# Optimization experiments

Measured on AMD Instinct MI355X. Metric: run time of the kernel, lower is better.

The kernel has to match this reference:

```python
import jax, jax.numpy as jnp
import numpy as np

N_DST = 50000
N_SRC = 50000
E = 800000
D = 128
R = 3
H_SEM = 128
NEG_SLOPE = 0.2  # DGL GATConv default


def setup_inputs() -> dict:
    key = jax.random.key(0)
    ks = jax.random.split(key, 40)
    s = 1.0 / np.sqrt(D)
    inp = {
        'dst_feat': jax.random.normal(ks[0], (N_DST, D), jnp.float32),
        'src_feat0': jax.random.normal(ks[1], (N_SRC, D), jnp.float32),
        'src_feat1': jax.random.normal(ks[2], (N_SRC, D), jnp.float32),
        'src_feat2': jax.random.normal(ks[3], (N_SRC, D), jnp.float32),
        'sem_W1': jax.random.normal(ks[4], (D, H_SEM), jnp.float32) * s,
        'sem_b1': jnp.zeros((H_SEM,), jnp.float32),
        'sem_W2': jax.random.normal(ks[5], (H_SEM, 1), jnp.float32) * (1.0 / np.sqrt(H_SEM)),
    }
    for r in range(R):
        inp[f'Wg{r}'] = jax.random.normal(ks[6 + r], (D, D), jnp.float32) * s
        inp[f'al{r}'] = jax.random.normal(ks[9 + r], (D,), jnp.float32) * s
        inp[f'ar{r}'] = jax.random.normal(ks[12 + r], (D,), jnp.float32) * s
        inp[f'bg{r}'] = jnp.zeros((D,), jnp.float32)
        inp[f'src_idx{r}'] = jax.random.randint(ks[15 + r], (E,), 0, N_SRC, jnp.int32)
        inp[f'dst_idx{r}'] = jax.random.randint(ks[18 + r], (E,), 0, N_DST, jnp.int32)
    return inp


def _gat(fs, fd, W, al, ar, b, sidx, didx):
    # DGL GATConv, num_heads=1, bipartite, eval mode (no dropout)
    hs = fs @ W                    # [Ns, D]
    hd = fd @ W                    # [Nd, D]
    el = hs @ al                   # [Ns]
    er = hd @ ar                   # [Nd]
    e = jax.nn.leaky_relu(el[sidx] + er[didx], NEG_SLOPE)  # [E]
    # edge softmax over incoming edges of each dst node
    m = jax.ops.segment_max(e, didx, num_segments=N_DST)
    a = jnp.exp(e - m[didx])
    z = jax.ops.segment_sum(a, didx, num_segments=N_DST)
    alpha = a / z[didx]            # [E]
    out = jax.ops.segment_sum(hs[sidx] * alpha[:, None], didx, num_segments=N_DST)
    return jax.nn.elu(out + b)     # [Nd, D]


def reference(dst_feat, src_feat0, src_feat1, src_feat2,
              Wg0, Wg1, Wg2, al0, al1, al2, ar0, ar1, ar2, bg0, bg1, bg2,
              sem_W1, sem_b1, sem_W2,
              src_idx0, src_idx1, src_idx2, dst_idx0, dst_idx1, dst_idx2):
    z0 = _gat(src_feat0, dst_feat, Wg0, al0, ar0, bg0, src_idx0, dst_idx0)
    z1 = _gat(src_feat1, dst_feat, Wg1, al1, ar1, bg1, src_idx1, dst_idx1)
    z2 = _gat(src_feat2, dst_feat, Wg2, al2, ar2, bg2, src_idx2, dst_idx2)
    z_m = jnp.stack([z0, z1, z2], axis=1)            # [N, R, D]
    h = jnp.tanh(z_m @ sem_W1 + sem_b1) @ sem_W2     # [N, R, 1]
    w = h.mean(axis=0)                               # [R, 1]
    a_w = jax.nn.softmax(w, axis=0)                  # [R, 1]
    z = (z_m * a_w[None, :, :]).sum(axis=1)          # [N, D]
    att_mp = a_w.squeeze()                           # [R]
    return (z, att_mp)
```

## Files before the change

kernel.cpp:

```cpp
#include <hip/hip_runtime.h>
#include <math.h>

#define D_DIM 128
#define N_DST 50000
#define N_SRC 50000
#define NE    800000
#define NEG_SLOPE 0.2f

#define NB        196
#define CAP       4608
#define CHUNK     8192
#define NBLK_REL  98
#define GEMM_BLKS 196
#define GEMM_GRID (3 * GEMM_BLKS)
#define ER_PB     86
#define SEM_GRID  512
#define SEM_TILES ((3 * N_DST + 63) / 64)

typedef unsigned short ushort_t;
using f32x4  = __attribute__((ext_vector_type(4))) float;
using bf16x8 = __attribute__((ext_vector_type(8))) short;

__device__ __forceinline__ ushort_t f2bf(float x) {
    unsigned u = __float_as_uint(x);
    unsigned r = (u + 0x7fffu + ((u >> 16) & 1u)) >> 16;
    return (ushort_t)r;
}
__device__ __forceinline__ float bf2f(ushort_t b) {
    return __uint_as_float(((unsigned)b) << 16);
}
__device__ __forceinline__ float bflo(unsigned u) { return __uint_as_float(u << 16); }
__device__ __forceinline__ float bfhi(unsigned u) { return __uint_as_float(u & 0xffff0000u); }
__device__ __forceinline__ float tanh_fast(float x) {
    float e = __expf(2.f * x);
    return 1.f - 2.f / (e + 1.f);
}

__device__ __forceinline__ void cvt8(float4 f0, float4 f1, bf16x8& hi, bf16x8& lo) {
    float f[8] = {f0.x, f0.y, f0.z, f0.w, f1.x, f1.y, f1.z, f1.w};
    #pragma unroll
    for (int i = 0; i < 8; i++) {
        ushort_t h = f2bf(f[i]);
        hi[i] = (short)h;
        lo[i] = (short)(ushort_t)(__float_as_uint(f[i] - bf2f(h)) >> 16);
    }
}

__global__ __launch_bounds__(256) void vecprep_kernel(
        const float* __restrict__ Wg0, const float* __restrict__ Wg1,
        const float* __restrict__ Wg2,
        const float* __restrict__ ar0, const float* __restrict__ ar1,
        const float* __restrict__ ar2,
        const float* __restrict__ W1,
        float* __restrict__ wv, ushort_t* __restrict__ Wt_g,
        ushort_t* __restrict__ Bv) {
    int bx = blockIdx.x, tid = threadIdx.x;
    if (bx < 3) {
        if (tid < 128) {
            const float* W  = bx == 0 ? Wg0 : (bx == 1 ? Wg1 : Wg2);
            const float* ar = bx == 0 ? ar0 : (bx == 1 ? ar1 : ar2);
            float sar = 0.f;
            for (int j = 0; j < D_DIM; j++) sar = fmaf(W[tid * D_DIM + j], ar[j], sar);
            wv[bx * D_DIM + tid] = sar;
        }
    } else if (bx < 67) {
        int idx = (bx - 3) * 256 + tid;
        int k = idx >> 7, n = idx & 127;
        Wt_g[n * 128 + k] = f2bf(W1[idx]);
    } else {
        int q = bx - 67;
        int rel = q >> 6;
        int idx = (q & 63) * 256 + tid;
        const float* W = rel == 0 ? Wg0 : (rel == 1 ? Wg1 : Wg2);
        int k = idx >> 7, n = idx & 127;
        float v = W[idx];
        ushort_t hi = f2bf(v);
        ushort_t lo = f2bf(v - bf2f(hi));
        int nt = n >> 4, l15 = n & 15;
        int kc = k >> 5, quad = (k >> 3) & 3, e = k & 7;
        int h2 = nt >> 2, n4 = nt & 3;
        int lane = quad * 16 + l15;
        int fh = kc * 16 + h2 * 8 + n4;
        ushort_t* dst = Bv + (size_t)rel * 32768;
        dst[(fh)     * 512 + lane * 8 + e] = hi;
        dst[(fh + 4) * 512 + lane * 8 + e] = lo;
    }
}

__global__ __launch_bounds__(256) void bucket_scatter_kernel(
        const int* __restrict__ d0, const int* __restrict__ d1, const int* __restrict__ d2,
        const int* __restrict__ s0, const int* __restrict__ s1, const int* __restrict__ s2,
        int* __restrict__ bucketCur, int2* __restrict__ pairs) {
    __shared__ int cnt[NB], base[NB], cur[NB];
    int bx = blockIdx.x;
    int r = bx / NBLK_REL, blk = bx % NBLK_REL;
    const int* dd = r == 0 ? d0 : (r == 1 ? d1 : d2);
    const int* ss = r == 0 ? s0 : (r == 1 ? s1 : s2);
    int tid = threadIdx.x;
    if (tid < NB) { cnt[tid] = 0; cur[tid] = 0; }
    __syncthreads();
    int e0 = blk * CHUNK, e1 = min(e0 + CHUNK, NE);
    for (int e = e0 + tid; e < e1; e += 256) atomicAdd(&cnt[dd[e] >> 8], 1);
    __syncthreads();
    if (tid < NB) base[tid] = cnt[tid] ? atomicAdd(&bucketCur[r * NB + tid], cnt[tid]) : 0;
    __syncthreads();
    for (int e = e0 + tid; e < e1; e += 256) {
        int d = dd[e], b = d >> 8;
        int rank = atomicAdd(&cur[b], 1);
        pairs[(size_t)(r * NB + b) * CAP + base[b] + rank] = make_int2(ss[e], d);
    }
}

__global__ __launch_bounds__(256) void csr_kernel(
        const int2* __restrict__ pairs, const int* __restrict__ bucketCur,
        int* __restrict__ offs, int* __restrict__ cnts, int* __restrict__ perm) {
    __shared__ int hist[256], sc[256], cur[256];
    int bx = blockIdx.x;
    int r = bx / NB, b = bx % NB;
    int tid = threadIdx.x;
    int nE = bucketCur[r * NB + b];
    size_t region = (size_t)(r * NB + b) * CAP;
    const int2* pr = pairs + region;
    hist[tid] = 0;
    __syncthreads();
    for (int i = tid; i < nE; i += 256) atomicAdd(&hist[pr[i].y & 255], 1);
    __syncthreads();
    int v = hist[tid];
    sc[tid] = v;
    __syncthreads();
    for (int off = 1; off < 256; off <<= 1) {
        int t = tid >= off ? sc[tid - off] : 0;
        __syncthreads();
        sc[tid] += t;
        __syncthreads();
    }
    int excl = sc[tid] - v;
    int dstg = b * 256 + tid;
    if (dstg < N_DST) { offs[r * N_DST + dstg] = (int)region + excl; cnts[r * N_DST + dstg] = v; }
    cur[tid] = excl;
    __syncthreads();
    int* pm = perm + region;
    for (int i = tid; i < nE; i += 256) {
        int2 p = pr[i];
        int rank = atomicAdd(&cur[p.y & 255], 1);
        pm[rank] = p.x;
    }
}

__global__ __launch_bounds__(512) void gemm_er_kernel(
        const float* __restrict__ A0, const float* __restrict__ A1, const float* __restrict__ A2,
        const ushort_t* __restrict__ Bv,
        const float* __restrict__ al0, const float* __restrict__ al1, const float* __restrict__ al2,
        const float* __restrict__ dstf, const float* __restrict__ wv,
        ushort_t* __restrict__ hs, float* __restrict__ elv) {
    __shared__ ushort_t Bs[32768];
    int bx = blockIdx.x;
    int rel = bx / GEMM_BLKS, blk = bx % GEMM_BLKS;
    const float* A  = rel == 0 ? A0 : (rel == 1 ? A1 : A2);
    const float* al = rel == 0 ? al0 : (rel == 1 ? al1 : al2);
    ushort_t* C = hs + (size_t)rel * N_SRC * 128;
    int tid = threadIdx.x;

    {
        const uint4* src = (const uint4*)(Bv + (size_t)rel * 32768);
        uint4* dl = (uint4*)Bs;
        #pragma unroll
        for (int i = 0; i < 8; i++) dl[tid + i * 512] = src[tid + i * 512];
    }

    int w = tid >> 6, lane = tid & 63;
    int quad = lane >> 4, l15 = lane & 15;
    int row0 = blk * 256 + w * 32;

    int gr0 = row0 + l15;      if (gr0 > N_SRC - 1) gr0 = N_SRC - 1;
    int gr1 = row0 + 16 + l15; if (gr1 > N_SRC - 1) gr1 = N_SRC - 1;
    const float* a0p = A + (size_t)gr0 * 128 + quad * 8;
    const float* a1p = A + (size_t)gr1 * 128 + quad * 8;

    float4 abuf[2][2][2];
    abuf[0][0][0] = *(const float4*)(a0p + 0);
    abuf[0][0][1] = *(const float4*)(a0p + 4);
    abuf[0][1][0] = *(const float4*)(a1p + 0);
    abuf[0][1][1] = *(const float4*)(a1p + 4);

    __syncthreads();

    f32x4 acc[2][8] = {};
    #pragma unroll
    for (int kc = 0; kc < 4; kc++) {
        const int par = kc & 1;
        if (kc < 3) {
            int ko = (kc + 1) * 32;
            abuf[par ^ 1][0][0] = *(const float4*)(a0p + ko);
            abuf[par ^ 1][0][1] = *(const float4*)(a0p + ko + 4);
            abuf[par ^ 1][1][0] = *(const float4*)(a1p + ko);
            abuf[par ^ 1][1][1] = *(const float4*)(a1p + ko + 4);
        }
        bf16x8 ah[2], alo[2];
        #pragma unroll
        for (int t = 0; t < 2; t++)
            cvt8(abuf[par][t][0], abuf[par][t][1], ah[t], alo[t]);

        #pragma unroll
        for (int h2 = 0; h2 < 2; h2++) {
            #pragma unroll
            for (int n4 = 0; n4 < 4; n4++) {
                int f = kc * 16 + h2 * 8 + n4;
                bf16x8 bh = *(const bf16x8*)&Bs[f * 512 + lane * 8];
                bf16x8 bl = *(const bf16x8*)&Bs[(f + 4) * 512 + lane * 8];
                int nt = h2 * 4 + n4;
                #pragma unroll
                for (int t = 0; t < 2; t++) {
                    acc[t][nt] = __builtin_amdgcn_mfma_f32_16x16x32_bf16(ah[t],  bh, acc[t][nt], 0, 0, 0);
                    acc[t][nt] = __builtin_amdgcn_mfma_f32_16x16x32_bf16(alo[t], bh, acc[t][nt], 0, 0, 0);
                    acc[t][nt] = __builtin_amdgcn_mfma_f32_16x16x32_bf16(ah[t],  bl, acc[t][nt], 0, 0, 0);
                }
            }
        }
    }

    float alv[8];
    #pragma unroll
    for (int nt = 0; nt < 8; nt++) alv[nt] = al[nt * 16 + l15];
    #pragma unroll
    for (int t = 0; t < 2; t++) {
        float part[4] = {0.f, 0.f, 0.f, 0.f};
        #pragma unroll
        for (int nt = 0; nt < 8; nt++)
            #pragma unroll
            for (int i = 0; i < 4; i++)
                part[i] = fmaf(acc[t][nt][i], alv[nt], part[i]);
        #pragma unroll
        for (int msk = 1; msk < 16; msk <<= 1)
            #pragma unroll
            for (int i = 0; i < 4; i++) part[i] += __shfl_xor(part[i], msk);
        if (l15 == 0) {
            #pragma unroll
            for (int i = 0; i < 4; i++) {
                int gr = row0 + t * 16 + quad * 4 + i;
                if (gr < N_SRC) elv[rel * N_DST + gr] = part[i];
            }
        }
    }

    int erbase = bx * ER_PB;
    float m0[11], m1[11];
    float wl0 = 0.f, wh0 = 0.f, wl1 = 0.f, wh1 = 0.f, wl2 = 0.f, wh2 = 0.f;
    int rend = 0;
    if (erbase < N_DST) {
        rend = min(erbase + ER_PB, N_DST);
        wl0 = wv[lane];       wh0 = wv[lane + 64];
        wl1 = wv[128 + lane]; wh1 = wv[128 + lane + 64];
        wl2 = wv[256 + lane]; wh2 = wv[256 + lane + 64];
        #pragma unroll
        for (int j = 0; j < 11; j++) {
            int r = erbase + w + 8 * j;
            int rr = r < rend ? r : erbase;
            m0[j] = dstf[(size_t)rr * 128 + lane];
            m1[j] = dstf[(size_t)rr * 128 + lane + 64];
        }
    }

    __syncthreads();

    ushort_t* Csh = Bs + w * 2304;
    #pragma unroll
    for (int h = 0; h < 2; h++) {
        __asm__ __volatile__("" ::: "memory");
        #pragma unroll
        for (int t = 0; t < 2; t++)
            #pragma unroll
            for (int ntl = 0; ntl < 4; ntl++) {
                int nt = h * 4 + ntl;
                #pragma unroll
                for (int i = 0; i < 4; i++)
                    Csh[(t * 16 + quad * 4 + i) * 72 + ntl * 16 + l15] = f2bf(acc[t][nt][i]);
            }
        __asm__ __volatile__("" ::: "memory");
        int r2 = lane >> 1, cb = (lane & 1) * 32;
        int gr = row0 + r2;
        if (gr < N_SRC) {
            ushort_t* dst = C + (size_t)gr * 128 + h * 64 + cb;
            #pragma unroll
            for (int k2 = 0; k2 < 4; k2++) {
                uint4 v = *(const uint4*)&Csh[r2 * 72 + cb + k2 * 8];
                *(uint4*)(dst + k2 * 8) = v;
            }
        }
    }

    if (erbase < N_DST) {
        #pragma unroll
        for (int j = 0; j < 11; j++) {
            int r = erbase + w + 8 * j;
            if (r < rend) {
                float p0 = fmaf(m0[j], wl0, m1[j] * wh0);
                float p1 = fmaf(m0[j], wl1, m1[j] * wh1);
                float p2 = fmaf(m0[j], wl2, m1[j] * wh2);
                #pragma unroll
                for (int off = 32; off > 0; off >>= 1) {
                    p0 += __shfl_down(p0, off);
                    p1 += __shfl_down(p1, off);
                    p2 += __shfl_down(p2, off);
                }
                if (lane == 0) {
                    elv[3 * N_DST + r] = p0;
                    elv[4 * N_DST + r] = p1;
                    elv[5 * N_DST + r] = p2;
                }
            }
        }
    }
}

__global__ __launch_bounds__(256) void aggregate_kernel(
        const ushort_t* __restrict__ hs, const float* __restrict__ elv,
        const int* __restrict__ perm, const int* __restrict__ offs,
        const int* __restrict__ cnts,
        const float* __restrict__ bg0, const float* __restrict__ bg1,
        const float* __restrict__ bg2, float* __restrict__ zm) {
    __shared__ int2 ew[4][2][64];
    int tid = threadIdx.x;
    int wave = tid >> 6, lane = tid & 63;
    int hw = lane >> 5, l31 = lane & 31;
    int bx  = blockIdx.x;
    int rel = bx / 6250;
    int b   = (bx % 6250) * 8 + wave * 2 + hw;
    const float* el  = elv + rel * N_DST;
    float erb = elv[(3 + rel) * N_DST + b];
    const float* bg = rel == 0 ? bg0 : (rel == 1 ? bg1 : bg2);
    const ushort_t* hsr = hs + (size_t)rel * N_SRC * 128;
    int o0 = offs[rel * N_DST + b], deg = cnts[rel * N_DST + b];
    float* zout = zm + ((size_t)b * 3 + rel) * 128;
    int2* ews = ew[wave][hw];

    if (deg <= 64) {
        int s0 = 0, s1 = 0;
        float e0 = 0.f, e1 = 0.f;
        if (l31 < deg) {
            s0 = perm[o0 + l31];
            float x = el[s0] + erb;
            x = x >= 0.f ? x : NEG_SLOPE * x;
            e0 = __expf(x);
        }
        if (deg > 32 && l31 + 32 < deg) {
            s1 = perm[o0 + l31 + 32];
            float x = el[s1] + erb;
            x = x >= 0.f ? x : NEG_SLOPE * x;
            e1 = __expf(x);
        }
        float lsum = e0 + e1;
        #pragma unroll
        for (int msk = 1; msk < 32; msk <<= 1) lsum += __shfl_xor(lsum, msk);
        float invz = deg > 0 ? 1.f / lsum : 0.f;

        ews[l31] = make_int2(s0 * 256, __float_as_int(e0 * invz));
        if (deg > 32)
            ews[l31 + 32] = make_int2(s1 * 256, __float_as_int(e1 * invz));
        __asm__ __volatile__("" ::: "memory");

        int degp = (deg + 3) & ~3;
        const char* basep = (const char*)hsr;
        int sub = l31 >> 4;
        int col16 = (l31 & 15) * 16;
        float a0 = 0.f, a1 = 0.f, a2 = 0.f, a3 = 0.f;
        float a4 = 0.f, a5 = 0.f, a6 = 0.f, a7 = 0.f;
        for (int j = 0; j < degp; j += 4) {
            int2 pA = ews[j + sub];
            int2 pB = ews[j + 2 + sub];
            uint4 hA = *(const uint4*)(basep + (unsigned)(pA.x + col16));
            uint4 hB = *(const uint4*)(basep + (unsigned)(pB.x + col16));
            float eA = __int_as_float(pA.y), eB = __int_as_float(pB.y);
            a0 = fmaf(eA, bflo(hA.x), a0); a1 = fmaf(eA, bfhi(hA.x), a1);
            a2 = fmaf(eA, bflo(hA.y), a2); a3 = fmaf(eA, bfhi(hA.y), a3);
            a4 = fmaf(eA, bflo(hA.z), a4); a5 = fmaf(eA, bfhi(hA.z), a5);
            a6 = fmaf(eA, bflo(hA.w), a6); a7 = fmaf(eA, bfhi(hA.w), a7);
            a0 = fmaf(eB, bflo(hB.x), a0); a1 = fmaf(eB, bfhi(hB.x), a1);
            a2 = fmaf(eB, bflo(hB.y), a2); a3 = fmaf(eB, bfhi(hB.y), a3);
            a4 = fmaf(eB, bflo(hB.z), a4); a5 = fmaf(eB, bfhi(hB.z), a5);
            a6 = fmaf(eB, bflo(hB.w), a6); a7 = fmaf(eB, bfhi(hB.w), a7);
        }
        a0 += __shfl_xor(a0, 16); a1 += __shfl_xor(a1, 16);
        a2 += __shfl_xor(a2, 16); a3 += __shfl_xor(a3, 16);
        a4 += __shfl_xor(a4, 16); a5 += __shfl_xor(a5, 16);
        a6 += __shfl_xor(a6, 16); a7 += __shfl_xor(a7, 16);
        if (sub == 0) {
            int c = (l31 & 15) * 8;
            float4 bgv0 = *(const float4*)&bg[c];
            float4 bgv1 = *(const float4*)&bg[c + 4];
            float4 z0, z1;
            z0.x = a0 + bgv0.x; z0.y = a1 + bgv0.y;
            z0.z = a2 + bgv0.z; z0.w = a3 + bgv0.w;
            z1.x = a4 + bgv1.x; z1.y = a5 + bgv1.y;
            z1.z = a6 + bgv1.z; z1.w = a7 + bgv1.w;
            z0.x = z0.x > 0.f ? z0.x : __expf(z0.x) - 1.f;
            z0.y = z0.y > 0.f ? z0.y : __expf(z0.y) - 1.f;
            z0.z = z0.z > 0.f ? z0.z : __expf(z0.z) - 1.f;
            z0.w = z0.w > 0.f ? z0.w : __expf(z0.w) - 1.f;
            z1.x = z1.x > 0.f ? z1.x : __expf(z1.x) - 1.f;
            z1.y = z1.y > 0.f ? z1.y : __expf(z1.y) - 1.f;
            z1.z = z1.z > 0.f ? z1.z : __expf(z1.z) - 1.f;
            z1.w = z1.w > 0.f ? z1.w : __expf(z1.w) - 1.f;
            *(float4*)&zout[c] = z0;
            *(float4*)&zout[c + 4] = z1;
        }
    } else {
        float lmax = -INFINITY;
        for (int i = l31; i < deg; i += 32) {
            int s = perm[o0 + i];
            float x = el[s] + erb;
            x = x >= 0.f ? x : NEG_SLOPE * x;
            lmax = fmaxf(lmax, x);
        }
        #pragma unroll
        for (int msk = 1; msk < 32; msk <<= 1) lmax = fmaxf(lmax, __shfl_xor(lmax, msk));
        float lsum = 0.f;
        for (int i = l31; i < deg; i += 32) {
            int s = perm[o0 + i];
            float x = el[s] + erb;
            x = x >= 0.f ? x : NEG_SLOPE * x;
            lsum += __expf(x - lmax);
        }
        #pragma unroll
        for (int msk = 1; msk < 32; msk <<= 1) lsum += __shfl_xor(lsum, msk);
        float invz = 1.f / lsum;
        float c0 = 0.f, c1 = 0.f, c2 = 0.f, c3 = 0.f;
        for (int j = 0; j < deg; j++) {
            int s = perm[o0 + j];
            float x = el[s] + erb;
            x = x >= 0.f ? x : NEG_SLOPE * x;
            float e_ = __expf(x - lmax) * invz;
            uint2 hv = *(const uint2*)(hsr + (size_t)s * 128 + l31 * 4);
            c0 = fmaf(e_, bflo(hv.x), c0);
            c1 = fmaf(e_, bfhi(hv.x), c1);
            c2 = fmaf(e_, bflo(hv.y), c2);
            c3 = fmaf(e_, bfhi(hv.y), c3);
        }
        int c = l31 * 4;
        float4 bgv = *(const float4*)&bg[c];
        float4 z;
        z.x = c0 + bgv.x; z.y = c1 + bgv.y;
        z.z = c2 + bgv.z; z.w = c3 + bgv.w;
        z.x = z.x > 0.f ? z.x : __expf(z.x) - 1.f;
        z.y = z.y > 0.f ? z.y : __expf(z.y) - 1.f;
        z.z = z.z > 0.f ? z.z : __expf(z.z) - 1.f;
        z.w = z.w > 0.f ? z.w : __expf(z.w) - 1.f;
        *(float4*)&zout[c] = z;
    }
}

__global__ __launch_bounds__(256) void semantic_kernel(
        const float* __restrict__ zm, const ushort_t* __restrict__ Wt_g,
        const float* __restrict__ b1, const float* __restrict__ W2,
        float* __restrict__ w_sum) {
    __shared__ ushort_t Wt[128 * 136];
    __shared__ float hsum[3];
    const int NROWS = N_DST * 3;
    int tid = threadIdx.x;
    if (tid < 3) hsum[tid] = 0.f;

    #pragma unroll
    for (int i = 0; i < 8; i++) {
        int c = i * 256 + tid;
        int n = c >> 4, c16 = c & 15;
        uint4 t = *(const uint4*)(Wt_g + n * 128 + c16 * 8);
        *(uint4*)&Wt[n * 136 + c16 * 8] = t;
    }
    __syncthreads();

    int w    = tid >> 6, lane = tid & 63;
    int quad = lane >> 4, l15 = lane & 15;
    float bb = b1[l15 * 8 + 0];

    for (int tile = blockIdx.x; tile < SEM_TILES; tile += gridDim.x) {
        long row0 = (long)tile * 64 + w * 16;
        long rA = row0 + l15; if (rA > NROWS - 1) rA = NROWS - 1;

        f32x4 acc[8] = {};
        #pragma unroll
        for (int kc = 0; kc < 4; kc++) {
            int k0 = kc * 32 + quad * 8;
            const float* src = zm + (size_t)rA * 128 + k0;
            float4 f0 = *(const float4*)src;
            float4 f1 = *(const float4*)(src + 4);
            bf16x8 a;
            a[0] = (short)f2bf(f0.x); a[1] = (short)f2bf(f0.y);
            a[2] = (short)f2bf(f0.z); a[3] = (short)f2bf(f0.w);
            a[4] = (short)f2bf(f1.x); a[5] = (short)f2bf(f1.y);
            a[6] = (short)f2bf(f1.z); a[7] = (short)f2bf(f1.w);
            #pragma unroll
            for (int nt = 0; nt < 8; nt++) {
                int n = nt * 16 + l15;
                bf16x8 bfr = *(const bf16x8*)&Wt[n * 136 + k0];
                acc[nt] = __builtin_amdgcn_mfma_f32_16x16x32_bf16(a, bfr, acc[nt], 0, 0, 0);
            }
        }

        float part[4] = {0.f, 0.f, 0.f, 0.f};
        #pragma unroll
        for (int nt = 0; nt < 8; nt++) {
            int n = nt * 16 + l15;
            float bbn = b1[n], ww = W2[n];
            #pragma unroll
            for (int i = 0; i < 4; i++) {
                float t = tanh_fast(acc[nt][i] + bbn);
                part[i] = fmaf(t, ww, part[i]);
            }
        }
        #pragma unroll
        for (int msk = 1; msk < 16; msk <<= 1)
            #pragma unroll
            for (int i = 0; i < 4; i++) part[i] += __shfl_xor(part[i], msk);
        if (l15 == 0) {
            #pragma unroll
            for (int i = 0; i < 4; i++) {
                long R = row0 + quad * 4 + i;
                if (R < NROWS) atomicAdd(&hsum[(int)(R % 3)], part[i]);
            }
        }
    }
    __syncthreads();
    if (tid < 3) atomicAdd(&w_sum[tid], hsum[tid]);
    (void)bb;
}

__global__ void combine_kernel(const float* __restrict__ zm, const float* __restrict__ w_sum,
                               float* __restrict__ out, float* __restrict__ out_att) {
    float w0 = w_sum[0] * (1.f / (float)N_DST);
    float w1 = w_sum[1] * (1.f / (float)N_DST);
    float w2 = w_sum[2] * (1.f / (float)N_DST);
    float m = fmaxf(w0, fmaxf(w1, w2));
    float e0 = __expf(w0 - m), e1 = __expf(w1 - m), e2 = __expf(w2 - m);
    float s = 1.f / (e0 + e1 + e2);
    float a0 = e0 * s, a1 = e1 * s, a2 = e2 * s;
    if (blockIdx.x == 0 && threadIdx.x < 3)
        out_att[threadIdx.x] = threadIdx.x == 0 ? a0 : (threadIdx.x == 1 ? a1 : a2);
    int id4 = blockIdx.x * 256 + threadIdx.x;
    int n  = id4 >> 5;
    int d4 = (id4 & 31) * 4;
    const float4 z0 = *(const float4*)&zm[((size_t)n * 3 + 0) * 128 + d4];
    const float4 z1 = *(const float4*)&zm[((size_t)n * 3 + 1) * 128 + d4];
    const float4 z2 = *(const float4*)&zm[((size_t)n * 3 + 2) * 128 + d4];
    float4 o;
    o.x = a0 * z0.x + a1 * z1.x + a2 * z2.x;
    o.y = a0 * z0.y + a1 * z1.y + a2 * z2.y;
    o.z = a0 * z0.z + a1 * z1.z + a2 * z2.z;
    o.w = a0 * z0.w + a1 * z1.w + a2 * z2.w;
    *(float4*)&out[(size_t)n * 128 + d4] = o;
}

extern "C" void kernel_launch(void* const* d_in, const int* in_sizes, int n_in,
                              void* d_out, int out_size, void* d_ws, size_t ws_size,
                              hipStream_t stream) {
    const float* dstf   = (const float*)d_in[0];
    const float* src0   = (const float*)d_in[1];
    const float* src1   = (const float*)d_in[2];
    const float* src2   = (const float*)d_in[3];
    const float* sem_W1 = (const float*)d_in[4];
    const float* sem_b1 = (const float*)d_in[5];
    const float* sem_W2 = (const float*)d_in[6];
    const float* Wg[3]  = {(const float*)d_in[7],  (const float*)d_in[13], (const float*)d_in[19]};
    const float* al[3]  = {(const float*)d_in[8],  (const float*)d_in[14], (const float*)d_in[20]};
    const float* ar[3]  = {(const float*)d_in[9],  (const float*)d_in[15], (const float*)d_in[21]};
    const float* bg[3]  = {(const float*)d_in[10], (const float*)d_in[16], (const float*)d_in[22]};
    const int*  sidx[3] = {(const int*)d_in[11], (const int*)d_in[17], (const int*)d_in[23]};
    const int*  didx[3] = {(const int*)d_in[12], (const int*)d_in[18], (const int*)d_in[24]};
    float* out = (float*)d_out;

    char* p = (char*)d_ws;
    auto alloc = [&](size_t bytes) -> char* {
        char* q = p; p += (bytes + 255) & ~(size_t)255; return q;
    };
    float*    zm   = (float*)alloc((size_t)N_DST * 3 * 128 * 4);
    ushort_t* hs   = (ushort_t*)alloc((size_t)3 * N_SRC * 128 * 2);
    float*    elv  = (float*)alloc((size_t)6 * N_DST * 4);
    float*    wv   = (float*)alloc((size_t)3 * 128 * 4);
    ushort_t* Wt_g = (ushort_t*)alloc((size_t)128 * 128 * 2);
    ushort_t* Bv   = (ushort_t*)alloc((size_t)3 * 32768 * 2);
    int* cnts = (int*)alloc((size_t)3 * N_DST * 4);
    int* offs = (int*)alloc((size_t)3 * N_DST * 4);
    int* perm = (int*)alloc((size_t)3 * NB * CAP * 4);
    int* zero = (int*)alloc((size_t)(3 * NB + 8) * 4);
    int*   bucketCur = zero;
    float* wsum      = (float*)(zero + 3 * NB);
    int2* pairs = (int2*)zm;

    hipMemsetAsync(zero, 0, (size_t)(3 * NB + 8) * 4, stream);

    vecprep_kernel<<<259, 256, 0, stream>>>(Wg[0], Wg[1], Wg[2], ar[0], ar[1], ar[2],
                                            sem_W1, wv, Wt_g, Bv);
    bucket_scatter_kernel<<<3 * NBLK_REL, 256, 0, stream>>>(didx[0], didx[1], didx[2],
                                                            sidx[0], sidx[1], sidx[2],
                                                            bucketCur, pairs);
    csr_kernel<<<3 * NB, 256, 0, stream>>>(pairs, bucketCur, offs, cnts, perm);
    gemm_er_kernel<<<GEMM_GRID, 512, 0, stream>>>(src0, src1, src2, Bv,
                                                  al[0], al[1], al[2],
                                                  dstf, wv, hs, elv);
    aggregate_kernel<<<3 * 6250, 256, 0, stream>>>(hs, elv, perm, offs, cnts,
                                                   bg[0], bg[1], bg[2], zm);
    semantic_kernel<<<SEM_GRID, 256, 0, stream>>>(zm, Wt_g, sem_b1, sem_W2, wsum);
    combine_kernel<<<6250, 256, 0, stream>>>(zm, wsum, out, out + (size_t)N_DST * 128);
}
```

Measured before the change: 417.7 us.

## Merge independent prep/scatter and CSR/GEMM kernels into shared launches

Combines the weight-prep and edge bucket-scatter kernels into one launch via block-index dispatch, and runs the CSR build blocks alongside the feature GEMM blocks in a single launch. This removes two kernel launch boundaries and lets independent work overlap on the GPU. The CSR path now runs with 512-thread blocks sharing the GEMM's LDS allocation, so its blocks carry the GEMM's large shared-memory footprint, which may limit occupancy.

```diff
diff --git a/kernel.cpp b/kernel.cpp
--- a/kernel.cpp
+++ b/kernel.cpp
@@ -13,6 +13,7 @@
 #define NBLK_REL  98
 #define GEMM_BLKS 196
 #define GEMM_GRID (3 * GEMM_BLKS)
+#define CSR_GRID  (3 * NB)
 #define ER_PB     86
 #define SEM_GRID  512
 #define SEM_TILES ((3 * N_DST + 63) / 64)
@@ -46,57 +47,56 @@
     }
 }
 
-__global__ __launch_bounds__(256) void vecprep_kernel(
+__global__ __launch_bounds__(256) void prep_scatter_kernel(
         const float* __restrict__ Wg0, const float* __restrict__ Wg1,
         const float* __restrict__ Wg2,
         const float* __restrict__ ar0, const float* __restrict__ ar1,
         const float* __restrict__ ar2,
         const float* __restrict__ W1,
         float* __restrict__ wv, ushort_t* __restrict__ Wt_g,
-        ushort_t* __restrict__ Bv) {
-    int bx = blockIdx.x, tid = threadIdx.x;
-    if (bx < 3) {
-        if (tid < 128) {
-            const float* W  = bx == 0 ? Wg0 : (bx == 1 ? Wg1 : Wg2);
-            const float* ar = bx == 0 ? ar0 : (bx == 1 ? ar1 : ar2);
-            float sar = 0.f;
-            for (int j = 0; j < D_DIM; j++) sar = fmaf(W[tid * D_DIM + j], ar[j], sar);
-            wv[bx * D_DIM + tid] = sar;
-        }
-    } else if (bx < 67) {
-        int idx = (bx - 3) * 256 + tid;
-        int k = idx >> 7, n = idx & 127;
-        Wt_g[n * 128 + k] = f2bf(W1[idx]);
-    } else {
-        int q = bx - 67;
-        int rel = q >> 6;
-        int idx = (q & 63) * 256 + tid;
-        const float* W = rel == 0 ? Wg0 : (rel == 1 ? Wg1 : Wg2);
-        int k = idx >> 7, n = idx & 127;
-        float v = W[idx];
-        ushort_t hi = f2bf(v);
-        ushort_t lo = f2bf(v - bf2f(hi));
-        int nt = n >> 4, l15 = n & 15;
-        int kc = k >> 5, quad = (k >> 3) & 3, e = k & 7;
-        int h2 = nt >> 2, n4 = nt & 3;
-        int lane = quad * 16 + l15;
-        int fh = kc * 16 + h2 * 8 + n4;
-        ushort_t* dst = Bv + (size_t)rel * 32768;
-        dst[(fh)     * 512 + lane * 8 + e] = hi;
-        dst[(fh + 4) * 512 + lane * 8 + e] = lo;
-    }
-}
-
-__global__ __launch_bounds__(256) void bucket_scatter_kernel(
+        ushort_t* __restrict__ Bv,
         const int* __restrict__ d0, const int* __restrict__ d1, const int* __restrict__ d2,
         const int* __restrict__ s0, const int* __restrict__ s1, const int* __restrict__ s2,
         int* __restrict__ bucketCur, int2* __restrict__ pairs) {
     __shared__ int cnt[NB], base[NB], cur[NB];
-    int bx = blockIdx.x;
-    int r = bx / NBLK_REL, blk = bx % NBLK_REL;
+    int bx = blockIdx.x, tid = threadIdx.x;
+    if (bx < 259) {
+        if (bx < 3) {
+            if (tid < 128) {
+                const float* W  = bx == 0 ? Wg0 : (bx == 1 ? Wg1 : Wg2);
+                const float* ar = bx == 0 ? ar0 : (bx == 1 ? ar1 : ar2);
+                float sar = 0.f;
+                for (int j = 0; j < D_DIM; j++) sar = fmaf(W[tid * D_DIM + j], ar[j], sar);
+                wv[bx * D_DIM + tid] = sar;
+            }
+        } else if (bx < 67) {
+            int idx = (bx - 3) * 256 + tid;
+            int k = idx >> 7, n = idx & 127;
+            Wt_g[n * 128 + k] = f2bf(W1[idx]);
+        } else {
+            int q = bx - 67;
+            int rel = q >> 6;
+            int idx = (q & 63) * 256 + tid;
+            const float* W = rel == 0 ? Wg0 : (rel == 1 ? Wg1 : Wg2);
+            int k = idx >> 7, n = idx & 127;
+            float v = W[idx];
+            ushort_t hi = f2bf(v);
+            ushort_t lo = f2bf(v - bf2f(hi));
+            int nt = n >> 4, l15 = n & 15;
+            int kc = k >> 5, quad = (k >> 3) & 3, e = k & 7;
+            int h2 = nt >> 2, n4 = nt & 3;
+            int lane = quad * 16 + l15;
+            int fh = kc * 16 + h2 * 8 + n4;
+            ushort_t* dst = Bv + (size_t)rel * 32768;
+            dst[(fh)     * 512 + lane * 8 + e] = hi;
+            dst[(fh + 4) * 512 + lane * 8 + e] = lo;
+        }
+        return;
+    }
+    int sb = bx - 259;
+    int r = sb / NBLK_REL, blk = sb % NBLK_REL;
     const int* dd = r == 0 ? d0 : (r == 1 ? d1 : d2);
     const int* ss = r == 0 ? s0 : (r == 1 ? s1 : s2);
-    int tid = threadIdx.x;
     if (tid < NB) { cnt[tid] = 0; cur[tid] = 0; }
     __syncthreads();
     int e0 = blk * CHUNK, e1 = min(e0 + CHUNK, NE);
@@ -111,55 +111,60 @@
     }
 }
 
-__global__ __launch_bounds__(256) void csr_kernel(
-        const int2* __restrict__ pairs, const int* __restrict__ bucketCur,
-        int* __restrict__ offs, int* __restrict__ cnts, int* __restrict__ perm) {
-    __shared__ int hist[256], sc[256], cur[256];
-    int bx = blockIdx.x;
-    int r = bx / NB, b = bx % NB;
-    int tid = threadIdx.x;
-    int nE = bucketCur[r * NB + b];
-    size_t region = (size_t)(r * NB + b) * CAP;
-    const int2* pr = pairs + region;
-    hist[tid] = 0;
-    __syncthreads();
-    for (int i = tid; i < nE; i += 256) atomicAdd(&hist[pr[i].y & 255], 1);
-    __syncthreads();
-    int v = hist[tid];
-    sc[tid] = v;
-    __syncthreads();
-    for (int off = 1; off < 256; off <<= 1) {
-        int t = tid >= off ? sc[tid - off] : 0;
-        __syncthreads();
-        sc[tid] += t;
-        __syncthreads();
-    }
-    int excl = sc[tid] - v;
-    int dstg = b * 256 + tid;
-    if (dstg < N_DST) { offs[r * N_DST + dstg] = (int)region + excl; cnts[r * N_DST + dstg] = v; }
-    cur[tid] = excl;
-    __syncthreads();
-    int* pm = perm + region;
-    for (int i = tid; i < nE; i += 256) {
-        int2 p = pr[i];
-        int rank = atomicAdd(&cur[p.y & 255], 1);
-        pm[rank] = p.x;
-    }
-}
-
-__global__ __launch_bounds__(512) void gemm_er_kernel(
+__global__ __launch_bounds__(512) void csr_gemm_kernel(
         const float* __restrict__ A0, const float* __restrict__ A1, const float* __restrict__ A2,
         const ushort_t* __restrict__ Bv,
         const float* __restrict__ al0, const float* __restrict__ al1, const float* __restrict__ al2,
         const float* __restrict__ dstf, const float* __restrict__ wv,
-        ushort_t* __restrict__ hs, float* __restrict__ elv) {
+        ushort_t* __restrict__ hs, float* __restrict__ elv,
+        const int2* __restrict__ pairs, const int* __restrict__ bucketCur,
+        int* __restrict__ offs, int* __restrict__ cnts, int* __restrict__ perm) {
     __shared__ ushort_t Bs[32768];
     int bx = blockIdx.x;
+    int tid = threadIdx.x;
+
+    if (bx >= GEMM_GRID) {
+        int cb = bx - GEMM_GRID;
+        int r = cb / NB, b = cb % NB;
+        int* hist = (int*)Bs;
+        int* sc   = hist + 256;
+        int* curc = hist + 512;
+        int nE = bucketCur[r * NB + b];
+        size_t region = (size_t)(r * NB + b) * CAP;
+        const int2* pr = pairs + region;
+        if (tid < 256) hist[tid] = 0;
+        __syncthreads();
+        for (int i = tid; i < nE; i += 512) atomicAdd(&hist[pr[i].y & 255], 1);
+        __syncthreads();
+        int v = 0;
+        if (tid < 256) { v = hist[tid]; sc[tid] = v; }
+        __syncthreads();
+        for (int off = 1; off < 256; off <<= 1) {
+            int t = (tid < 256 && tid >= off) ? sc[tid - off] : 0;
+            __syncthreads();
+            if (tid < 256) sc[tid] += t;
+            __syncthreads();
+        }
+        if (tid < 256) {
+            int excl = sc[tid] - v;
+            int dstg = b * 256 + tid;
+            if (dstg < N_DST) { offs[r * N_DST + dstg] = (int)region + excl; cnts[r * N_DST + dstg] = v; }
+            curc[tid] = excl;
+        }
+        __syncthreads();
+        int* pm = perm + region;
+        for (int i = tid; i < nE; i += 512) {
+            int2 p = pr[i];
+            int rank = atomicAdd(&curc[p.y & 255], 1);
+            pm[rank] = p.x;
+        }
+        return;
+    }
+
     int rel = bx / GEMM_BLKS, blk = bx % GEMM_BLKS;
     const float* A  = rel == 0 ? A0 : (rel == 1 ? A1 : A2);
     const float* al = rel == 0 ? al0 : (rel == 1 ? al1 : al2);
     ushort_t* C = hs + (size_t)rel * N_SRC * 128;
-    int tid = threadIdx.x;
 
     {
         const uint4* src = (const uint4*)(Bv + (size_t)rel * 32768);
@@ -277,13 +282,13 @@
                     Csh[(t * 16 + quad * 4 + i) * 72 + ntl * 16 + l15] = f2bf(acc[t][nt][i]);
             }
         __asm__ __volatile__("" ::: "memory");
-        int r2 = lane >> 1, cb = (lane & 1) * 32;
+        int r2 = lane >> 1, cb2 = (lane & 1) * 32;
         int gr = row0 + r2;
         if (gr < N_SRC) {
-            ushort_t* dst = C + (size_t)gr * 128 + h * 64 + cb;
+            ushort_t* dst = C + (size_t)gr * 128 + h * 64 + cb2;
             #pragma unroll
             for (int k2 = 0; k2 < 4; k2++) {
-                uint4 v = *(const uint4*)&Csh[r2 * 72 + cb + k2 * 8];
+                uint4 v = *(const uint4*)&Csh[r2 * 72 + cb2 + k2 * 8];
                 *(uint4*)(dst + k2 * 8) = v;
             }
         }
@@ -470,7 +475,6 @@
 
     int w    = tid >> 6, lane = tid & 63;
     int quad = lane >> 4, l15 = lane & 15;
-    float bb = b1[l15 * 8 + 0];
 
     for (int tile = blockIdx.x; tile < SEM_TILES; tile += gridDim.x) {
         long row0 = (long)tile * 64 + w * 16;
@@ -521,7 +525,6 @@
     }
     __syncthreads();
     if (tid < 3) atomicAdd(&w_sum[tid], hsum[tid]);
-    (void)bb;
 }
 
 __global__ void combine_kernel(const float* __restrict__ zm, const float* __restrict__ w_sum,
@@ -587,15 +590,12 @@
 
     hipMemsetAsync(zero, 0, (size_t)(3 * NB + 8) * 4, stream);
 
-    vecprep_kernel<<<259, 256, 0, stream>>>(Wg[0], Wg[1], Wg[2], ar[0], ar[1], ar[2],
-                                            sem_W1, wv, Wt_g, Bv);
-    bucket_scatter_kernel<<<3 * NBLK_REL, 256, 0, stream>>>(didx[0], didx[1], didx[2],
-                                                            sidx[0], sidx[1], sidx[2],
-                                                            bucketCur, pairs);
-    csr_kernel<<<3 * NB, 256, 0, stream>>>(pairs, bucketCur, offs, cnts, perm);
-    gemm_er_kernel<<<GEMM_GRID, 512, 0, stream>>>(src0, src1, src2, Bv,
-                                                  al[0], al[1], al[2],
-                                                  dstf, wv, hs, elv);
+    prep_scatter_kernel<<<259 + 3 * NBLK_REL, 256, 0, stream>>>(
+        Wg[0], Wg[1], Wg[2], ar[0], ar[1], ar[2], sem_W1, wv, Wt_g, Bv,
+        didx[0], didx[1], didx[2], sidx[0], sidx[1], sidx[2], bucketCur, pairs);
+    csr_gemm_kernel<<<GEMM_GRID + CSR_GRID, 512, 0, stream>>>(
+        src0, src1, src2, Bv, al[0], al[1], al[2], dstf, wv, hs, elv,
+        pairs, bucketCur, offs, cnts, perm);
     aggregate_kernel<<<3 * 6250, 256, 0, stream>>>(hs, elv, perm, offs, cnts,
                                                    bg[0], bg[1], bg[2], zm);
     semantic_kernel<<<SEM_GRID, 256, 0, stream>>>(zm, Wt_g, sem_b1, sem_W2, wsum);
```

New measurement: 397.2 us. -4.9%, faster.
